# Kernel tuning notes

Measured on AMD Instinct MI355X. Metric: run time of the kernel, lower is better.

Reference implementation:

```python
import jax, jax.numpy as jnp
import numpy as np

HID = 128
NUM_LAYERS = 3
B = 256
ND, ED, SD = 16384, 65536, 131072
NP_, EP, SP = 131072, 524288, 524288


def setup_inputs():
    key = jax.random.key(0)
    ks = jax.random.split(key, 40)
    r = lambda i, sh: jax.random.normal(ks[i], sh, jnp.float32) * 0.05
    ri = lambda i, sh, hi: jax.random.randint(ks[i], sh, 0, hi, jnp.int32)
    return {
        'drug_x': r(0, (ND, 78)),
        'prot_x': r(1, (NP_, 70)),
        'd_feature': r(2, (B, HID)),
        'p_feature': r(3, (B, HID)),
        'drug_edge_index': ri(4, (2, ED), ND),
        'drug_batch': jnp.sort(ri(5, (ND,), B)),
        'drug_sub_node': ri(6, (SD,), ND),
        'drug_sub_ind': ri(7, (SD,), ND),
        'prot_edge_index': ri(8, (2, EP), NP_),
        'prot_batch': jnp.sort(ri(9, (NP_,), B)),
        'prot_sub_node': ri(10, (SP,), NP_),
        'prot_sub_ind': ri(11, (SP,), NP_),
        'enc_Wd': r(12, (78, HID)), 'enc_bd': r(13, (HID,)),
        'enc_Wp': r(14, (70, HID)), 'enc_bp': r(15, (HID,)),
        'convW_d': r(16, (NUM_LAYERS, HID, HID)), 'convb_d': r(17, (NUM_LAYERS, HID)),
        'convW_p': r(18, (NUM_LAYERS, HID, HID)), 'convb_p': r(19, (NUM_LAYERS, HID)),
        'bng_d': jnp.ones((NUM_LAYERS, HID), jnp.float32), 'bnb_d': jnp.zeros((NUM_LAYERS, HID), jnp.float32),
        'bng_p': jnp.ones((NUM_LAYERS, HID), jnp.float32), 'bnb_p': jnp.zeros((NUM_LAYERS, HID), jnp.float32),
        'vn_emb_d': r(20, (HID,)), 'vn_emb_p': r(21, (HID,)),
        'vnW_d': r(22, (NUM_LAYERS - 1, HID, HID)), 'vnb_d': r(23, (NUM_LAYERS - 1, HID)),
        'vnW_p': r(24, (NUM_LAYERS - 1, HID, HID)), 'vnb_p': r(25, (NUM_LAYERS - 1, HID)),
        'mlpd1_W': r(26, (2 * HID, HID)), 'mlpd1_b': r(27, (HID,)),
        'mlpd1_g': jnp.ones((HID,), jnp.float32), 'mlpd1_be': jnp.zeros((HID,), jnp.float32),
        'mlpp1_W': r(28, (2 * HID, HID)), 'mlpp1_b': r(29, (HID,)),
        'mlpp1_g': jnp.ones((HID,), jnp.float32), 'mlpp1_be': jnp.zeros((HID,), jnp.float32),
    }


def _bn(x, g, b):
    # training-mode batch norm (batch statistics)
    m = jnp.mean(x, 0)
    v = jnp.var(x, 0)
    return (x - m) * jax.lax.rsqrt(v + 1e-5) * g + b


def _seg_mean(x, ids, n):
    s = jax.ops.segment_sum(x, ids, num_segments=n)
    c = jax.ops.segment_sum(jnp.ones((x.shape[0],), x.dtype), ids, num_segments=n)
    return s / jnp.maximum(c, 1.0)[:, None]


def _gcn(h, W, b, ei, n):
    # PyG GCNConv: sym-normalized A+I, then linear
    src, dst = ei[0], ei[1]
    hw = h @ W
    deg = jax.ops.segment_sum(jnp.ones((src.shape[0],), h.dtype), dst, num_segments=n) + 1.0
    nrm = jax.lax.rsqrt(deg)
    msg = hw[src] * (nrm[src] * nrm[dst])[:, None]  # [E, HID]
    return jax.ops.segment_sum(msg, dst, num_segments=n) + hw * (nrm * nrm)[:, None] + b


def _forward(fl, ints):
    (drug_x, prot_x, d_feature, p_feature, enc_Wd, enc_bd, enc_Wp, enc_bp,
     convW_d, convb_d, convW_p, convb_p, bng_d, bnb_d, bng_p, bnb_p,
     vn_emb_d, vn_emb_p, vnW_d, vnb_d, vnW_p, vnb_p,
     mlpd1_W, mlpd1_b, mlpd1_g, mlpd1_be, mlpp1_W, mlpp1_b, mlpp1_g, mlpp1_be) = fl
    (d_ei, d_batch, d_sn, d_si, p_ei, p_batch, p_sn, p_si) = ints
    Nd, Npn = drug_x.shape[0], prot_x.shape[0]
    Bn = d_feature.shape[0]
    hd = drug_x @ enc_Wd + enc_bd
    hp = prot_x @ enc_Wp + enc_bp
    # virtual node init: learned embedding + pretrained fingerprint feature
    vx_d = vn_emb_d[None, :] + d_feature  # [B, HID]
    vx_p = vn_emb_p[None, :] + p_feature
    for i in range(NUM_LAYERS):
        # virtual-node broadcast -> GCN -> BN -> ReLU (dropout off / eval)
        hd = _gcn(hd + vx_d[d_batch], convW_d[i], convb_d[i], d_ei, Nd)
        hp = _gcn(hp + vx_p[p_batch], convW_p[i], convb_p[i], p_ei, Npn)
        hd = jax.nn.relu(_bn(hd, bng_d[i], bnb_d[i]))
        hp = jax.nn.relu(_bn(hp, bng_p[i], bnb_p[i]))
        # k-hop subgraph structure extraction (scatter_mean back to nodes)
        hd_struct = _seg_mean(hd[d_sn], d_si, Nd)
        hp_struct = _seg_mean(hp[p_sn], p_si, Npn)
        if i < NUM_LAYERS - 1:
            vx_d = vx_d + jax.nn.relu((jax.ops.segment_sum(hd_struct, d_batch, num_segments=Bn) + vx_d) @ vnW_d[i] + vnb_d[i])
            vx_p = vx_p + jax.nn.relu((jax.ops.segment_sum(hp_struct, p_batch, num_segments=Bn) + vx_p) @ vnW_p[i] + vnb_p[i])
    # cross-modal sync: broadcast pooled drug info onto protein nodes & vice versa
    sync_drug = hp_struct + _seg_mean(hd_struct, d_batch, Bn)[p_batch]  # [Np, HID]
    sync_prot = hd_struct + _seg_mean(hp_struct, p_batch, Bn)[d_batch]  # [Nd, HID]
    final_drug = _bn(jnp.concatenate([_seg_mean(sync_prot, d_batch, Bn), d_feature], 1) @ mlpd1_W + mlpd1_b, mlpd1_g, mlpd1_be)
    final_prot = _bn(jnp.concatenate([_seg_mean(sync_drug, p_batch, Bn), p_feature], 1) @ mlpp1_W + mlpp1_b, mlpp1_g, mlpp1_be)
    return final_drug, final_prot


def reference(drug_x, prot_x, d_feature, p_feature, drug_edge_index, drug_batch,
              drug_sub_node, drug_sub_ind, prot_edge_index, prot_batch,
              prot_sub_node, prot_sub_ind, enc_Wd, enc_bd, enc_Wp, enc_bp,
              convW_d, convb_d, convW_p, convb_p, bng_d, bnb_d, bng_p, bnb_p,
              vn_emb_d, vn_emb_p, vnW_d, vnb_d, vnW_p, vnb_p,
              mlpd1_W, mlpd1_b, mlpd1_g, mlpd1_be, mlpp1_W, mlpp1_b, mlpp1_g, mlpp1_be):
    fl = (drug_x, prot_x, d_feature, p_feature, enc_Wd, enc_bd, enc_Wp, enc_bp,
          convW_d, convb_d, convW_p, convb_p, bng_d, bnb_d, bng_p, bnb_p,
          vn_emb_d, vn_emb_p, vnW_d, vnb_d, vnW_p, vnb_p,
          mlpd1_W, mlpd1_b, mlpd1_g, mlpd1_be, mlpp1_W, mlpp1_b, mlpp1_g, mlpp1_be)
    ints = (drug_edge_index, drug_batch, drug_sub_node, drug_sub_ind,
            prot_edge_index, prot_batch, prot_sub_node, prot_sub_ind)
    return _forward(fl, ints)
```

## Files before the change

### kernel.cpp

```cpp
#include <hip/hip_runtime.h>
#include <cstdint>
#include <cstddef>

#define HID 128

using bf16x8 = __attribute__((ext_vector_type(8))) short;
using f32x4v = __attribute__((ext_vector_type(4))) float;

static __device__ __forceinline__ unsigned short f2b(float x) {
  unsigned int u = __float_as_uint(x);
  unsigned int r = u + 0x7FFFu + ((u >> 16) & 1u);
  return (unsigned short)(r >> 16);
}
static __device__ __forceinline__ float b2f(unsigned short h) {
  return __uint_as_float(((unsigned int)h) << 16);
}

static __device__ __forceinline__ int lowerb(const int* __restrict__ a, int n, int v) {
  int lo = 0, hi = n;
  while (lo < hi) { int m = (lo + hi) >> 1; if (a[m] < v) lo = m + 1; else hi = m; }
  return lo;
}

__global__ void k_hist_all(const int* i0, int n0, int* c0, const int* i1, int n1, int* c1,
                           const int* i2, int n2, int* c2, const int* i3, int n3, int* c3) {
  const int seg = blockIdx.x & 3;
  const int lb = blockIdx.x >> 2;
  const int stride = (gridDim.x >> 2) * blockDim.x;
  const int start = lb * blockDim.x + threadIdx.x;
  const int* idx = seg == 0 ? i0 : seg == 1 ? i1 : seg == 2 ? i2 : i3;
  int* cnt = seg == 0 ? c0 : seg == 1 ? c1 : seg == 2 ? c2 : c3;
  const int n = seg == 0 ? n0 : seg == 1 ? n1 : seg == 2 ? n2 : n3;
  for (int i = start; i < n; i += stride) atomicAdd(&cnt[idx[i]], 1);
}

__global__ void k_nrm_nb(const int* __restrict__ deg_d, float* __restrict__ nrm_d, int ND,
                         const int* __restrict__ deg_p, float* __restrict__ nrm_p, int NP,
                         const int* __restrict__ d_batch, float* __restrict__ nb_d,
                         const int* __restrict__ p_batch, float* __restrict__ nb_p, int B) {
  const int stride = gridDim.x * blockDim.x;
  const int total = ND + NP + 2 * B;
  for (int i = blockIdx.x * blockDim.x + threadIdx.x; i < total; i += stride) {
    if (i < ND) nrm_d[i] = rsqrtf((float)deg_d[i] + 1.0f);
    else if (i < ND + NP) { const int j = i - ND; nrm_p[j] = rsqrtf((float)deg_p[j] + 1.0f); }
    else if (i < ND + NP + B) {
      const int b = i - ND - NP;
      nb_d[b] = (float)(lowerb(d_batch, ND, b + 1) - lowerb(d_batch, ND, b));
    } else {
      const int b = i - ND - NP - B;
      nb_p[b] = (float)(lowerb(p_batch, NP, b + 1) - lowerb(p_batch, NP, b));
    }
  }
}

__global__ __launch_bounds__(256)
void k_scan1_all(const int* c0, int* r0, int n0, int nb0,
                 const int* c1, int* r1, int n1, int nb1,
                 const int* c2, int* r2, int n2, int nb2,
                 const int* c3, int* r3, int n3, int nb3, int* aux) {
  __shared__ int sh[256];
  int b = blockIdx.x, seg = 0;
  if (b >= nb0) { b -= nb0; seg = 1; }
  if (seg == 1 && b >= nb1) { b -= nb1; seg = 2; }
  if (seg == 2 && b >= nb2) { b -= nb2; seg = 3; }
  const int* cnt = seg == 0 ? c0 : seg == 1 ? c1 : seg == 2 ? c2 : c3;
  int* row = seg == 0 ? r0 : seg == 1 ? r1 : seg == 2 ? r2 : r3;
  const int n = seg == 0 ? n0 : seg == 1 ? n1 : seg == 2 ? n2 : n3;
  const int tid = threadIdx.x;
  const int base = b * 1024 + tid * 4;
  int v0 = base + 0 < n ? cnt[base + 0] : 0;
  int v1 = base + 1 < n ? cnt[base + 1] : 0;
  int v2 = base + 2 < n ? cnt[base + 2] : 0;
  int v3 = base + 3 < n ? cnt[base + 3] : 0;
  const int s = v0 + v1 + v2 + v3;
  sh[tid] = s;
  __syncthreads();
  for (int o = 1; o < 256; o <<= 1) {
    const int t = (tid >= o) ? sh[tid - o] : 0;
    __syncthreads();
    sh[tid] += t;
    __syncthreads();
  }
  int excl = sh[tid] - s;
  if (tid == 255) aux[seg * 256 + b] = sh[255];
  if (base + 0 < n) row[base + 0] = excl; excl += v0;
  if (base + 1 < n) row[base + 1] = excl; excl += v1;
  if (base + 2 < n) row[base + 2] = excl; excl += v2;
  if (base + 3 < n) row[base + 3] = excl;
}

__global__ __launch_bounds__(256)
void k_scan2_all(int* aux, int nb0, int nb1, int nb2, int nb3) {
  __shared__ int sh[256];
  const int seg = blockIdx.x;
  const int nb = seg == 0 ? nb0 : seg == 1 ? nb1 : seg == 2 ? nb2 : nb3;
  int* a = aux + seg * 256;
  const int tid = threadIdx.x;
  const int v = tid < nb ? a[tid] : 0;
  sh[tid] = v;
  __syncthreads();
  for (int o = 1; o < 256; o <<= 1) {
    const int t = (tid >= o) ? sh[tid - o] : 0;
    __syncthreads();
    sh[tid] += t;
    __syncthreads();
  }
  if (tid < nb) a[tid] = sh[tid] - v;
}

__global__ __launch_bounds__(256)
void k_scan3_all(int* r0, int n0, int nb0, int t0, int* r1, int n1, int nb1, int t1,
                 int* r2, int n2, int nb2, int t2, int* r3, int n3, int nb3, int t3,
                 const int* aux) {
  int b = blockIdx.x, seg = 0;
  if (b >= nb0) { b -= nb0; seg = 1; }
  if (seg == 1 && b >= nb1) { b -= nb1; seg = 2; }
  if (seg == 2 && b >= nb2) { b -= nb2; seg = 3; }
  int* row = seg == 0 ? r0 : seg == 1 ? r1 : seg == 2 ? r2 : r3;
  const int n = seg == 0 ? n0 : seg == 1 ? n1 : seg == 2 ? n2 : n3;
  const int total = seg == 0 ? t0 : seg == 1 ? t1 : seg == 2 ? t2 : t3;
  const int add = aux[seg * 256 + b];
  const int base = b * 1024 + threadIdx.x * 4;
  #pragma unroll
  for (int k = 0; k < 4; ++k)
    if (base + k < n) row[base + k] += add;
  if (b == 0 && threadIdx.x == 0) row[n] = total;
}

__global__ void k_fill_all(const int* p_src, const int* p_dst, const int* rowE_p, int* curE_p,
                           int* colE_p, float* cofE_p, const float* nrm_p, int EP,
                           const int* d_src, const int* d_dst, const int* rowE_d, int* curE_d,
                           int* colE_d, float* cofE_d, const float* nrm_d, int ED,
                           const int* p_sn, const int* p_si, const int* rowS_p, int* curS_p,
                           int* colS_p, int SP,
                           const int* d_sn, const int* d_si, const int* rowS_d, int* curS_d,
                           int* colS_d, int SD) {
  const int seg = blockIdx.x & 3;
  const int lb = blockIdx.x >> 2;
  const int stride = (gridDim.x >> 2) * blockDim.x;
  const int start = lb * blockDim.x + threadIdx.x;
  if (seg == 0) {
    for (int e = start; e < EP; e += stride) {
      const int d = p_dst[e], s = p_src[e];
      const int pos = rowE_p[d] + atomicAdd(&curE_p[d], 1);
      colE_p[pos] = s;
      cofE_p[pos] = nrm_p[s] * nrm_p[d];
    }
  } else if (seg == 1) {
    for (int e = start; e < ED; e += stride) {
      const int d = d_dst[e], s = d_src[e];
      const int pos = rowE_d[d] + atomicAdd(&curE_d[d], 1);
      colE_d[pos] = s;
      cofE_d[pos] = nrm_d[s] * nrm_d[d];
    }
  } else if (seg == 2) {
    for (int j = start; j < SP; j += stride) {
      const int t = p_si[j];
      const int pos = rowS_p[t] + atomicAdd(&curS_p[t], 1);
      colS_p[pos] = p_sn[j];
    }
  } else {
    for (int j = start; j < SD; j += stride) {
      const int t = d_si[j];
      const int pos = rowS_d[t] + atomicAdd(&curS_d[t], 1);
      colS_d[pos] = d_sn[j];
    }
  }
}

__global__ void k_vx_init_both(const float* __restrict__ emb_d, const float* __restrict__ d_feat,
                               float* __restrict__ vx_d, const float* __restrict__ emb_p,
                               const float* __restrict__ p_feat, float* __restrict__ vx_p,
                               int half) {
  const int stride = gridDim.x * blockDim.x;
  for (int i = blockIdx.x * blockDim.x + threadIdx.x; i < 2 * half; i += stride) {
    if (i < half) vx_d[i] = emb_d[i & (HID - 1)] + d_feat[i];
    else { const int j = i - half; vx_p[j] = emb_p[j & (HID - 1)] + p_feat[j]; }
  }
}

__global__ __launch_bounds__(256)
void k_wcvt_all(const float* __restrict__ convW_d, const float* __restrict__ convW_p,
                const float* __restrict__ enc_Wd, const float* __restrict__ enc_Wp,
                unsigned short* __restrict__ WhiAll, unsigned short* __restrict__ WloAll) {
  const int seg = blockIdx.x >> 5;
  const int lb = blockIdx.x & 31;
  const float* W;
  int K;
  if (seg < 3) { W = convW_d + (size_t)seg * HID * HID; K = 128; }
  else if (seg < 6) { W = convW_p + (size_t)(seg - 3) * HID * HID; K = 128; }
  else if (seg == 6) { W = enc_Wd; K = 78; }
  else { W = enc_Wp; K = 70; }
  unsigned short* Whi = WhiAll + (size_t)seg * HID * HID;
  unsigned short* Wlo = WloAll + (size_t)seg * HID * HID;
  for (int i = lb * 256 + threadIdx.x; i < HID * HID; i += 32 * 256) {
    const int c = i >> 7, k = i & 127;
    const float v = (k < K) ? W[k * HID + c] : 0.f;
    const unsigned short hi = f2b(v);
    Whi[i] = hi;
    Wlo[i] = f2b(v - b2f(hi));
  }
}

__global__ void k_xcvt_both(const float* __restrict__ Xd, int Kd, unsigned short* __restrict__ Dhi,
                            unsigned short* __restrict__ Dlo, int totD,
                            const float* __restrict__ Xp, int Kp, unsigned short* __restrict__ Phi,
                            unsigned short* __restrict__ Plo, int totP) {
  const int stride = gridDim.x * blockDim.x;
  for (int i = blockIdx.x * blockDim.x + threadIdx.x; i < totD + totP; i += stride) {
    if (i < totD) {
      const int node = i >> 7, k = i & 127;
      const float v = (k < Kd) ? Xd[(size_t)node * Kd + k] : 0.f;
      const unsigned short hi = f2b(v);
      Dhi[i] = hi;
      Dlo[i] = f2b(v - b2f(hi));
    } else {
      const int j = i - totD;
      const int node = j >> 7, k = j & 127;
      const float v = (k < Kp) ? Xp[(size_t)node * Kp + k] : 0.f;
      const unsigned short hi = f2b(v);
      Phi[j] = hi;
      Plo[j] = f2b(v - b2f(hi));
    }
  }
}

template<bool ENC>
__global__ __launch_bounds__(256, 2)
void k_gemm_both(const unsigned short* __restrict__ Zhi0, const unsigned short* __restrict__ Zlo0,
                 const unsigned short* __restrict__ Whi0, const unsigned short* __restrict__ Wlo0,
                 const float* __restrict__ bias0, float* __restrict__ G0, int nbk0,
                 const unsigned short* __restrict__ Zhi1, const unsigned short* __restrict__ Zlo1,
                 const unsigned short* __restrict__ Whi1, const unsigned short* __restrict__ Wlo1,
                 const float* __restrict__ bias1, float* __restrict__ G1,
                 float* __restrict__ stats_sl) {
  __shared__ unsigned short Bt[128 * 132];
  __shared__ float lstats[256];
  const int bid = blockIdx.x;
  const bool isP = bid >= nbk0;
  const int lb = isP ? bid - nbk0 : bid;
  const unsigned short* Zhi = isP ? Zhi1 : Zhi0;
  const unsigned short* Zlo = isP ? Zlo1 : Zlo0;
  const unsigned short* Wthi = isP ? Whi1 : Whi0;
  const unsigned short* Wtlo = isP ? Wlo1 : Wlo0;
  const float* bias = isP ? bias1 : bias0;
  float* G = isP ? G1 : G0;

  const int tid = threadIdx.x;
  const int w = tid >> 6;
  const int l = tid & 63;
  const int l15 = l & 15;
  const int kb = l >> 4;

  for (int i = tid; i < 128 * 16; i += 256) {
    const int c = i >> 4, k8 = i & 15;
    *(bf16x8*)(&Bt[c * 132 + k8 * 8]) = *(const bf16x8*)(Wthi + (size_t)c * 128 + k8 * 8);
  }
  if constexpr (!ENC) lstats[tid] = 0.f;

  const int rbase = lb * 128 + w * 32 + l15;
  bf16x8 ahi[2][4], alo[2][4];
  #pragma unroll
  for (int rt = 0; rt < 2; ++rt)
    #pragma unroll
    for (int ks = 0; ks < 4; ++ks) {
      ahi[rt][ks] = *(const bf16x8*)(Zhi + (size_t)(rbase + rt * 16) * 128 + ks * 32 + kb * 8);
      alo[rt][ks] = *(const bf16x8*)(Zlo + (size_t)(rbase + rt * 16) * 128 + ks * 32 + kb * 8);
    }

  f32x4v acc[2][8];
  #pragma unroll
  for (int rt = 0; rt < 2; ++rt)
    #pragma unroll
    for (int ct = 0; ct < 8; ++ct)
      acc[rt][ct] = (f32x4v){0.f, 0.f, 0.f, 0.f};

  __syncthreads();
  #pragma unroll
  for (int ks = 0; ks < 4; ++ks) {
    #pragma unroll
    for (int ct = 0; ct < 8; ++ct) {
      const bf16x8 b = *(const bf16x8*)(&Bt[(ct * 16 + l15) * 132 + ks * 32 + kb * 8]);
      acc[0][ct] = __builtin_amdgcn_mfma_f32_16x16x32_bf16(ahi[0][ks], b, acc[0][ct], 0, 0, 0);
      acc[1][ct] = __builtin_amdgcn_mfma_f32_16x16x32_bf16(ahi[1][ks], b, acc[1][ct], 0, 0, 0);
      acc[0][ct] = __builtin_amdgcn_mfma_f32_16x16x32_bf16(alo[0][ks], b, acc[0][ct], 0, 0, 0);
      acc[1][ct] = __builtin_amdgcn_mfma_f32_16x16x32_bf16(alo[1][ks], b, acc[1][ct], 0, 0, 0);
    }
  }
  __syncthreads();

  for (int i = tid; i < 128 * 16; i += 256) {
    const int c = i >> 4, k8 = i & 15;
    *(bf16x8*)(&Bt[c * 132 + k8 * 8]) = *(const bf16x8*)(Wtlo + (size_t)c * 128 + k8 * 8);
  }
  __syncthreads();
  #pragma unroll
  for (int ks = 0; ks < 4; ++ks) {
    #pragma unroll
    for (int ct = 0; ct < 8; ++ct) {
      const bf16x8 b = *(const bf16x8*)(&Bt[(ct * 16 + l15) * 132 + ks * 32 + kb * 8]);
      acc[0][ct] = __builtin_amdgcn_mfma_f32_16x16x32_bf16(ahi[0][ks], b, acc[0][ct], 0, 0, 0);
      acc[1][ct] = __builtin_amdgcn_mfma_f32_16x16x32_bf16(ahi[1][ks], b, acc[1][ct], 0, 0, 0);
    }
  }

  float bb[8];
  if constexpr (ENC) {
    #pragma unroll
    for (int ct = 0; ct < 8; ++ct) bb[ct] = bias[ct * 16 + l15];
  }
  float csum[8], csq[8];
  #pragma unroll
  for (int ct = 0; ct < 8; ++ct) { csum[ct] = 0.f; csq[ct] = 0.f; }
  #pragma unroll
  for (int rt = 0; rt < 2; ++rt) {
    const size_t grow = (size_t)lb * 128 + w * 32 + rt * 16 + (l >> 4) * 4;
    #pragma unroll
    for (int j = 0; j < 4; ++j) {
      float* gr = G + (grow + j) * 128 + l15;
      #pragma unroll
      for (int ct = 0; ct < 8; ++ct) {
        float v = acc[rt][ct][j];
        if constexpr (ENC) v += bb[ct];
        gr[ct * 16] = v;
        if constexpr (!ENC) { csum[ct] += v; csq[ct] += v * v; }
      }
    }
  }
  if constexpr (!ENC) {
    #pragma unroll
    for (int ct = 0; ct < 8; ++ct) {
      csum[ct] += __shfl_xor(csum[ct], 16);
      csum[ct] += __shfl_xor(csum[ct], 32);
      csq[ct] += __shfl_xor(csq[ct], 16);
      csq[ct] += __shfl_xor(csq[ct], 32);
    }
    if (l < 16) {
      #pragma unroll
      for (int ct = 0; ct < 8; ++ct) {
        atomicAdd(&lstats[ct * 16 + l], csum[ct]);
        atomicAdd(&lstats[128 + ct * 16 + l], csq[ct]);
      }
    }
    __syncthreads();
    const int slice = (isP ? 32 : 0) + (lb & 31);
    atomicAdd(&stats_sl[(size_t)slice * 256 + tid], lstats[tid]);
  }
}

__global__ __launch_bounds__(128)
void k_bn_scale_both(float* __restrict__ stats_sl,
                     const float* g0, const float* b0, float invN0, float* scsh0,
                     const float* g1, const float* b1, float invN1, float* scsh1) {
  const int seg = blockIdx.x;
  float* base = stats_sl + (size_t)seg * 32 * 256;
  const float* g = seg ? g1 : g0;
  const float* bb = seg ? b1 : b0;
  const float invN = seg ? invN1 : invN0;
  float* scsh = seg ? scsh1 : scsh0;
  const int c = threadIdx.x;
  float s = 0.f, ss = 0.f;
  for (int k = 0; k < 32; ++k) {
    s += base[(size_t)k * 256 + c];
    ss += base[(size_t)k * 256 + 128 + c];
    base[(size_t)k * 256 + c] = 0.f;
    base[(size_t)k * 256 + 128 + c] = 0.f;
  }
  const float m = s * invN;
  const float var = ss * invN - m * m;
  const float sc = g[c] * rsqrtf(var + 1e-5f);
  scsh[c] = sc;
  scsh[HID + c] = bb[c] - m * sc;
}

template<bool HASF>
__global__ __launch_bounds__(256)
void k_agg_both(const int* rE0, const int* cE0, const float* wE0, const float* G0,
                const float* scsh0, const int* bat0, const float* vx0, const float* nrm0,
                unsigned short* Zhi0, unsigned short* Zlo0, int nbk0,
                const int* rE1, const int* cE1, const float* wE1, const float* G1,
                const float* scsh1, const int* bat1, const float* vx1, const float* nrm1,
                unsigned short* Zhi1, unsigned short* Zlo1) {
  const int bid = blockIdx.x;
  const bool isP = bid >= nbk0;
  const int lb = isP ? bid - nbk0 : bid;
  const int* rowp = isP ? rE1 : rE0;
  const int* colp = isP ? cE1 : cE0;
  const float* coefp = isP ? wE1 : wE0;
  const float* G = isP ? G1 : G0;
  const float* scsh = isP ? scsh1 : scsh0;
  const int* batch = isP ? bat1 : bat0;
  const float* vx = isP ? vx1 : vx0;
  const float* nrm = isP ? nrm1 : nrm0;
  unsigned short* Zhi = isP ? Zhi1 : Zhi0;
  unsigned short* Zlo = isP ? Zlo1 : Zlo0;

  const int tid = threadIdx.x;
  const int node = lb * 8 + (tid >> 5);
  const int c4 = tid & 31;
  float4 sc, shv;
  if constexpr (HASF) {
    sc = ((const float4*)scsh)[c4];
    shv = ((const float4*)(scsh + HID))[c4];
  }
  auto loadU = [&](int i) -> float4 {
    float4 v = *(const float4*)(G + (size_t)i * HID + c4 * 4);
    if constexpr (HASF) {
      v.x = fmaxf(v.x * sc.x + shv.x, 0.f);
      v.y = fmaxf(v.y * sc.y + shv.y, 0.f);
      v.z = fmaxf(v.z * sc.z + shv.z, 0.f);
      v.w = fmaxf(v.w * sc.w + shv.w, 0.f);
    }
    const float4 u = *(const float4*)(vx + (size_t)batch[i] * HID + c4 * 4);
    v.x += u.x; v.y += u.y; v.z += u.z; v.w += u.w;
    return v;
  };
  const int lo = rowp[node], hi = rowp[node + 1];
  const float nv = nrm[node];
  const float s2 = nv * nv;
  float4 acc = loadU(node);
  acc.x *= s2; acc.y *= s2; acc.z *= s2; acc.w *= s2;
  int e = lo;
  for (; e + 4 <= hi; e += 4) {
    const float w0 = coefp[e], w1 = coefp[e + 1], w2 = coefp[e + 2], w3 = coefp[e + 3];
    const float4 v0 = loadU(colp[e]);
    const float4 v1 = loadU(colp[e + 1]);
    const float4 v2 = loadU(colp[e + 2]);
    const float4 v3 = loadU(colp[e + 3]);
    acc.x += v0.x * w0 + v1.x * w1 + v2.x * w2 + v3.x * w3;
    acc.y += v0.y * w0 + v1.y * w1 + v2.y * w2 + v3.y * w3;
    acc.z += v0.z * w0 + v1.z * w1 + v2.z * w2 + v3.z * w3;
    acc.w += v0.w * w0 + v1.w * w1 + v2.w * w2 + v3.w * w3;
  }
  for (; e < hi; ++e) {
    const float w = coefp[e];
    const float4 v = loadU(colp[e]);
    acc.x += v.x * w; acc.y += v.y * w; acc.z += v.z * w; acc.w += v.w * w;
  }
  ushort4 h, lo4;
  h.x = f2b(acc.x); lo4.x = f2b(acc.x - b2f(h.x));
  h.y = f2b(acc.y); lo4.y = f2b(acc.y - b2f(h.y));
  h.z = f2b(acc.z); lo4.z = f2b(acc.z - b2f(h.z));
  h.w = f2b(acc.w); lo4.w = f2b(acc.w - b2f(h.w));
  *(ushort4*)(Zhi + (size_t)node * HID + c4 * 4) = h;
  *(ushort4*)(Zlo + (size_t)node * HID + c4 * 4) = lo4;
}

__global__ __launch_bounds__(256)
void k_sub_pool_both(const int* rS0, const int* cS0, const float* G0, const float* scsh0,
                     const int* bat0, float* sumS0, int nbk0,
                     const int* rS1, const int* cS1, const float* G1, const float* scsh1,
                     const int* bat1, float* sumS1) {
  __shared__ float sh[8][HID];
  __shared__ int batl[8];
  const int bid = blockIdx.x;
  const bool isP = bid >= nbk0;
  const int lb = isP ? bid - nbk0 : bid;
  const int* rowp = isP ? rS1 : rS0;
  const int* colp = isP ? cS1 : cS0;
  const float* G = isP ? G1 : G0;
  const float* scsh = isP ? scsh1 : scsh0;
  const int* batch = isP ? bat1 : bat0;
  float* sumS = isP ? sumS1 : sumS0;

  const int tid = threadIdx.x;
  const int grp = tid >> 5;
  const int node = lb * 8 + grp;
  const int c4 = tid & 31;
  const float4 sc = ((const float4*)scsh)[c4];
  const float4 shv = ((const float4*)(scsh + HID))[c4];
  const int lo = rowp[node], hi = rowp[node + 1];
  float4 acc = {0.f, 0.f, 0.f, 0.f};
  int e = lo;
  for (; e + 4 <= hi; e += 4) {
    const int i0 = colp[e], i1 = colp[e + 1], i2 = colp[e + 2], i3 = colp[e + 3];
    const float4 v0 = *(const float4*)(G + (size_t)i0 * HID + c4 * 4);
    const float4 v1 = *(const float4*)(G + (size_t)i1 * HID + c4 * 4);
    const float4 v2 = *(const float4*)(G + (size_t)i2 * HID + c4 * 4);
    const float4 v3 = *(const float4*)(G + (size_t)i3 * HID + c4 * 4);
    acc.x += fmaxf(v0.x * sc.x + shv.x, 0.f) + fmaxf(v1.x * sc.x + shv.x, 0.f)
           + fmaxf(v2.x * sc.x + shv.x, 0.f) + fmaxf(v3.x * sc.x + shv.x, 0.f);
    acc.y += fmaxf(v0.y * sc.y + shv.y, 0.f) + fmaxf(v1.y * sc.y + shv.y, 0.f)
           + fmaxf(v2.y * sc.y + shv.y, 0.f) + fmaxf(v3.y * sc.y + shv.y, 0.f);
    acc.z += fmaxf(v0.z * sc.z + shv.z, 0.f) + fmaxf(v1.z * sc.z + shv.z, 0.f)
           + fmaxf(v2.z * sc.z + shv.z, 0.f) + fmaxf(v3.z * sc.z + shv.z, 0.f);
    acc.w += fmaxf(v0.w * sc.w + shv.w, 0.f) + fmaxf(v1.w * sc.w + shv.w, 0.f)
           + fmaxf(v2.w * sc.w + shv.w, 0.f) + fmaxf(v3.w * sc.w + shv.w, 0.f);
  }
  for (; e < hi; ++e) {
    const float4 v = *(const float4*)(G + (size_t)colp[e] * HID + c4 * 4);
    acc.x += fmaxf(v.x * sc.x + shv.x, 0.f);
    acc.y += fmaxf(v.y * sc.y + shv.y, 0.f);
    acc.z += fmaxf(v.z * sc.z + shv.z, 0.f);
    acc.w += fmaxf(v.w * sc.w + shv.w, 0.f);
  }
  const float inv = 1.0f / fmaxf((float)(hi - lo), 1.0f);
  acc.x *= inv; acc.y *= inv; acc.z *= inv; acc.w *= inv;
  ((float4*)&sh[grp][0])[c4] = acc;
  if (tid < 8) batl[tid] = batch[lb * 8 + tid];
  __syncthreads();
  if (tid < HID) {
    int cur = batl[0];
    float a = 0.f;
    #pragma unroll
    for (int g = 0; g < 8; ++g) {
      if (batl[g] != cur) {
        atomicAdd(&sumS[(size_t)cur * HID + tid], a);
        a = 0.f;
        cur = batl[g];
      }
      a += sh[g][tid];
    }
    atomicAdd(&sumS[(size_t)cur * HID + tid], a);
  }
}

__global__ __launch_bounds__(128)
void k_vn_update_both(const float* ps0, float* vx0, const float* W0, const float* b0,
                      const float* ps1, float* vx1, const float* W1, const float* b1, int B) {
  const int gb = blockIdx.x;
  const bool isP = gb >= B;
  const int b = isP ? gb - B : gb;
  const float* pooledSum = isP ? ps1 : ps0;
  float* vx = isP ? vx1 : vx0;
  const float* W = isP ? W1 : W0;
  const float* bias = isP ? b1 : b0;
  const int c = threadIdx.x;
  __shared__ float xin[HID];
  xin[c] = pooledSum[(size_t)b * HID + c] + vx[(size_t)b * HID + c];
  __syncthreads();
  float acc = bias[c];
  #pragma unroll 8
  for (int k = 0; k < HID; k += 4) {
    const float4 x = *(const float4*)&xin[k];
    acc += x.x * W[k * HID + c] + x.y * W[(k + 1) * HID + c]
         + x.z * W[(k + 2) * HID + c] + x.w * W[(k + 3) * HID + c];
  }
  vx[(size_t)b * HID + c] += fmaxf(acc, 0.0f);
}

__global__ __launch_bounds__(128)
void k_final_A(const float* __restrict__ sum_Sd, const float* __restrict__ sum_Sp,
               const float* __restrict__ nb_d, const float* __restrict__ nb_p,
               float* __restrict__ A_d, float* __restrict__ A_p) {
  const int b = blockIdx.x, c = threadIdx.x;
  const float nd = nb_d[b], np_ = nb_p[b];
  const float md = sum_Sd[(size_t)b * HID + c] / fmaxf(nd, 1.f);
  const float mp = sum_Sp[(size_t)b * HID + c] / fmaxf(np_, 1.f);
  A_d[(size_t)b * HID + c] = md + (nd > 0.f ? mp : 0.f);
  A_p[(size_t)b * HID + c] = mp + (np_ > 0.f ? md : 0.f);
}

__global__ __launch_bounds__(128)
void k_final_mlp_both(const float* A0, const float* f0, const float* W0, const float* b0,
                      const float* A1, const float* f1, const float* W1, const float* b1,
                      float* __restrict__ fpre, int B) {
  const int gb = blockIdx.x;
  const bool isP = gb >= B;
  const int b = isP ? gb - B : gb;
  const float* A = isP ? A1 : A0;
  const float* feat = isP ? f1 : f0;
  const float* W = isP ? W1 : W0;
  const float* bias = isP ? b1 : b0;
  const int c = threadIdx.x;
  __shared__ float xin[2 * HID];
  xin[c] = A[(size_t)b * HID + c];
  xin[HID + c] = feat[(size_t)b * HID + c];
  __syncthreads();
  float acc = bias[c];
  #pragma unroll 8
  for (int k = 0; k < 2 * HID; k += 4) {
    const float4 x = *(const float4*)&xin[k];
    acc += x.x * W[k * HID + c] + x.y * W[(k + 1) * HID + c]
         + x.z * W[(k + 2) * HID + c] + x.w * W[(k + 3) * HID + c];
  }
  fpre[(size_t)gb * HID + c] = acc;
}

__global__ __launch_bounds__(256)
void k_bn_stats_both(const float* __restrict__ fpre, float* __restrict__ statsF, int B) {
  __shared__ float sh[2][256];
  const int seg = blockIdx.x >= 128 ? 1 : 0;
  const int lb = blockIdx.x - seg * 128;
  const float* X = fpre + (size_t)seg * B * HID;
  float* stats = statsF + seg * 256;
  const int tid = threadIdx.x;
  const int c = tid & (HID - 1);
  const int half = tid >> 7;
  float s = 0.f, ss = 0.f;
  for (int r = lb * 2 + half; r < B; r += 256) {
    const float v = X[(size_t)r * HID + c];
    s += v; ss += v * v;
  }
  sh[0][tid] = s; sh[1][tid] = ss;
  __syncthreads();
  if (tid < HID) {
    atomicAdd(&stats[c], sh[0][tid] + sh[0][tid + 128]);
    atomicAdd(&stats[HID + c], sh[1][tid] + sh[1][tid + 128]);
  }
}

__global__ void k_bn_apply_both(const float* __restrict__ fpre, float* __restrict__ out,
                                const float* __restrict__ statsF,
                                const float* g0, const float* b0,
                                const float* g1, const float* b1, int B, float invN) {
  const int stride = gridDim.x * blockDim.x;
  const int n4 = 2 * B * 32;
  for (int i = blockIdx.x * blockDim.x + threadIdx.x; i < n4; i += stride) {
    const int seg = i >= B * 32 ? 1 : 0;
    const int c4 = i & 31;
    const float* stats = statsF + seg * 256;
    const float4 m4 = ((const float4*)stats)[c4];
    const float4 q4 = ((const float4*)stats)[32 + c4];
    const float4 g4 = ((const float4*)(seg ? g1 : g0))[c4];
    const float4 b4 = ((const float4*)(seg ? b1 : b0))[c4];
    float4 v = ((const float4*)fpre)[i];
    float m, va;
    m = m4.x * invN; va = q4.x * invN - m * m; v.x = (v.x - m) * rsqrtf(va + 1e-5f) * g4.x + b4.x;
    m = m4.y * invN; va = q4.y * invN - m * m; v.y = (v.y - m) * rsqrtf(va + 1e-5f) * g4.y + b4.y;
    m = m4.z * invN; va = q4.z * invN - m * m; v.z = (v.z - m) * rsqrtf(va + 1e-5f) * g4.z + b4.z;
    m = m4.w * invN; va = q4.w * invN - m * m; v.w = (v.w - m) * rsqrtf(va + 1e-5f) * g4.w + b4.w;
    ((float4*)out)[i] = v;
  }
}

extern "C" void kernel_launch(void* const* d_in, const int* in_sizes, int n_in,
                              void* d_out, int out_size, void* d_ws, size_t ws_size,
                              hipStream_t stream) {
  const float* drug_x   = (const float*)d_in[0];
  const float* prot_x   = (const float*)d_in[1];
  const float* d_feat   = (const float*)d_in[2];
  const float* p_feat   = (const float*)d_in[3];
  const int*   d_ei     = (const int*)d_in[4];
  const int*   d_batch  = (const int*)d_in[5];
  const int*   d_sn     = (const int*)d_in[6];
  const int*   d_si     = (const int*)d_in[7];
  const int*   p_ei     = (const int*)d_in[8];
  const int*   p_batch  = (const int*)d_in[9];
  const int*   p_sn     = (const int*)d_in[10];
  const int*   p_si     = (const int*)d_in[11];
  const float* enc_Wd   = (const float*)d_in[12];
  const float* enc_bd   = (const float*)d_in[13];
  const float* enc_Wp   = (const float*)d_in[14];
  const float* enc_bp   = (const float*)d_in[15];
  const float* convW_d  = (const float*)d_in[16];
  const float* convW_p  = (const float*)d_in[18];
  const float* bng_d    = (const float*)d_in[20];
  const float* bnb_d    = (const float*)d_in[21];
  const float* bng_p    = (const float*)d_in[22];
  const float* bnb_p    = (const float*)d_in[23];
  const float* vn_emb_d = (const float*)d_in[24];
  const float* vn_emb_p = (const float*)d_in[25];
  const float* vnW_d    = (const float*)d_in[26];
  const float* vnb_d    = (const float*)d_in[27];
  const float* vnW_p    = (const float*)d_in[28];
  const float* vnb_p    = (const float*)d_in[29];
  const float* mlpd1_W  = (const float*)d_in[30];
  const float* mlpd1_b  = (const float*)d_in[31];
  const float* mlpd1_g  = (const float*)d_in[32];
  const float* mlpd1_be = (const float*)d_in[33];
  const float* mlpp1_W  = (const float*)d_in[34];
  const float* mlpp1_b  = (const float*)d_in[35];
  const float* mlpp1_g  = (const float*)d_in[36];
  const float* mlpp1_be = (const float*)d_in[37];

  const int ND = in_sizes[5];
  const int ED = in_sizes[4] / 2;
  const int SD = in_sizes[6];
  const int NP = in_sizes[9];
  const int EP = in_sizes[8] / 2;
  const int SP = in_sizes[10];
  const int B  = in_sizes[2] / HID;
  (void)n_in; (void)out_size; (void)ws_size;

  char* wsb = (char*)d_ws;
  size_t off = 0;
  auto alloc = [&](size_t bytes) -> void* {
    void* p = (void*)(wsb + off);
    off = (off + bytes + 255) & ~(size_t)255;
    return p;
  };
  float* Gp = (float*)alloc((size_t)NP * HID * 4);
  unsigned short* Zhi_p = (unsigned short*)alloc((size_t)NP * HID * 2);
  unsigned short* Zlo_p = (unsigned short*)alloc((size_t)NP * HID * 2);
  float* Gd = (float*)alloc((size_t)ND * HID * 4);
  unsigned short* Zhi_d = (unsigned short*)alloc((size_t)ND * HID * 2);
  unsigned short* Zlo_d = (unsigned short*)alloc((size_t)ND * HID * 2);
  unsigned short* WhiAll = (unsigned short*)alloc((size_t)8 * HID * HID * 2);
  unsigned short* WloAll = (unsigned short*)alloc((size_t)8 * HID * HID * 2);
  float* nrm_p = (float*)alloc((size_t)NP * 4);
  float* nrm_d = (float*)alloc((size_t)ND * 4);
  int* rowE_p = (int*)alloc((size_t)(NP + 1) * 4);
  int* rowE_d = (int*)alloc((size_t)(ND + 1) * 4);
  int* rowS_p = (int*)alloc((size_t)(NP + 1) * 4);
  int* rowS_d = (int*)alloc((size_t)(ND + 1) * 4);
  int* colE_p = (int*)alloc((size_t)EP * 4);
  float* cofE_p = (float*)alloc((size_t)EP * 4);
  int* colE_d = (int*)alloc((size_t)ED * 4);
  float* cofE_d = (float*)alloc((size_t)ED * 4);
  int* colS_p = (int*)alloc((size_t)SP * 4);
  int* colS_d = (int*)alloc((size_t)SD * 4);
  int* aux    = (int*)alloc(4 * 256 * 4);
  float* vx_d  = (float*)alloc((size_t)B * HID * 4);
  float* vx_p  = (float*)alloc((size_t)B * HID * 4);
  float* sum_Sd = (float*)alloc((size_t)B * HID * 4);
  float* sum_Sp = (float*)alloc((size_t)B * HID * 4);
  float* A_d   = (float*)alloc((size_t)B * HID * 4);
  float* A_p   = (float*)alloc((size_t)B * HID * 4);
  float* nb_d  = (float*)alloc((size_t)B * 4);
  float* nb_p  = (float*)alloc((size_t)B * 4);
  float* scsh_d = (float*)alloc(2 * HID * 4);
  float* scsh_p = (float*)alloc(2 * HID * 4);
  float* fpre  = (float*)alloc((size_t)2 * B * HID * 4);
  float* statsF = (float*)alloc(2 * 256 * 4);
  const size_t zstart = off;
  int* deg_p  = (int*)alloc((size_t)NP * 4);
  int* deg_d  = (int*)alloc((size_t)ND * 4);
  int* scnt_p = (int*)alloc((size_t)NP * 4);
  int* scnt_d = (int*)alloc((size_t)ND * 4);
  int* curE_p = (int*)alloc((size_t)NP * 4);
  int* curE_d = (int*)alloc((size_t)ND * 4);
  int* curS_p = (int*)alloc((size_t)NP * 4);
  int* curS_d = (int*)alloc((size_t)ND * 4);
  float* stats_sl = (float*)alloc((size_t)64 * 256 * 4);
  const size_t zend = off;

  const int* d_src = d_ei;  const int* d_dst = d_ei + ED;
  const int* p_src = p_ei;  const int* p_dst = p_ei + EP;

  hipMemsetAsync(wsb + zstart, 0, zend - zstart, stream);
  k_hist_all<<<4096, 256, 0, stream>>>(p_dst, EP, deg_p, d_dst, ED, deg_d,
                                       p_si, SP, scnt_p, d_si, SD, scnt_d);
  k_nrm_nb<<<1024, 256, 0, stream>>>(deg_d, nrm_d, ND, deg_p, nrm_p, NP,
                                     d_batch, nb_d, p_batch, nb_p, B);
  const int nbP = (NP + 1023) / 1024, nbD = (ND + 1023) / 1024;
  k_scan1_all<<<2 * nbP + 2 * nbD, 256, 0, stream>>>(
      deg_p, rowE_p, NP, nbP, deg_d, rowE_d, ND, nbD,
      scnt_p, rowS_p, NP, nbP, scnt_d, rowS_d, ND, nbD, aux);
  k_scan2_all<<<4, 256, 0, stream>>>(aux, nbP, nbD, nbP, nbD);
  k_scan3_all<<<2 * nbP + 2 * nbD, 256, 0, stream>>>(
      rowE_p, NP, nbP, EP, rowE_d, ND, nbD, ED,
      rowS_p, NP, nbP, SP, rowS_d, ND, nbD, SD, aux);
  k_fill_all<<<4096, 256, 0, stream>>>(
      p_src, p_dst, rowE_p, curE_p, colE_p, cofE_p, nrm_p, EP,
      d_src, d_dst, rowE_d, curE_d, colE_d, cofE_d, nrm_d, ED,
      p_sn, p_si, rowS_p, curS_p, colS_p, SP,
      d_sn, d_si, rowS_d, curS_d, colS_d, SD);

  k_wcvt_all<<<256, 256, 0, stream>>>(convW_d, convW_p, enc_Wd, enc_Wp, WhiAll, WloAll);
  k_xcvt_both<<<4096, 256, 0, stream>>>(drug_x, 78, Zhi_d, Zlo_d, ND * HID,
                                        prot_x, 70, Zhi_p, Zlo_p, NP * HID);
  k_gemm_both<true><<<ND / 128 + NP / 128, 256, 0, stream>>>(
      Zhi_d, Zlo_d, WhiAll + (size_t)6 * HID * HID, WloAll + (size_t)6 * HID * HID,
      enc_bd, Gd, ND / 128,
      Zhi_p, Zlo_p, WhiAll + (size_t)7 * HID * HID, WloAll + (size_t)7 * HID * HID,
      enc_bp, Gp, nullptr);
  k_vx_init_both<<<128, 256, 0, stream>>>(vn_emb_d, d_feat, vx_d, vn_emb_p, p_feat, vx_p, B * HID);

  for (int l = 0; l < 3; ++l) {
    if (l == 0)
      k_agg_both<false><<<ND / 8 + NP / 8, 256, 0, stream>>>(
          rowE_d, colE_d, cofE_d, Gd, nullptr, d_batch, vx_d, nrm_d, Zhi_d, Zlo_d, ND / 8,
          rowE_p, colE_p, cofE_p, Gp, nullptr, p_batch, vx_p, nrm_p, Zhi_p, Zlo_p);
    else
      k_agg_both<true><<<ND / 8 + NP / 8, 256, 0, stream>>>(
          rowE_d, colE_d, cofE_d, Gd, scsh_d, d_batch, vx_d, nrm_d, Zhi_d, Zlo_d, ND / 8,
          rowE_p, colE_p, cofE_p, Gp, scsh_p, p_batch, vx_p, nrm_p, Zhi_p, Zlo_p);
    k_gemm_both<false><<<ND / 128 + NP / 128, 256, 0, stream>>>(
        Zhi_d, Zlo_d, WhiAll + (size_t)l * HID * HID, WloAll + (size_t)l * HID * HID,
        nullptr, Gd, ND / 128,
        Zhi_p, Zlo_p, WhiAll + (size_t)(3 + l) * HID * HID, WloAll + (size_t)(3 + l) * HID * HID,
        nullptr, Gp, stats_sl);
    k_bn_scale_both<<<2, 128, 0, stream>>>(stats_sl,
        bng_d + l * HID, bnb_d + l * HID, 1.0f / (float)ND, scsh_d,
        bng_p + l * HID, bnb_p + l * HID, 1.0f / (float)NP, scsh_p);
    hipMemsetAsync(sum_Sd, 0, (size_t)2 * B * HID * 4, stream);
    k_sub_pool_both<<<ND / 8 + NP / 8, 256, 0, stream>>>(
        rowS_d, colS_d, Gd, scsh_d, d_batch, sum_Sd, ND / 8,
        rowS_p, colS_p, Gp, scsh_p, p_batch, sum_Sp);
    if (l < 2)
      k_vn_update_both<<<2 * B, 128, 0, stream>>>(
          sum_Sd, vx_d, vnW_d + (size_t)l * HID * HID, vnb_d + l * HID,
          sum_Sp, vx_p, vnW_p + (size_t)l * HID * HID, vnb_p + l * HID, B);
  }

  k_final_A<<<B, 128, 0, stream>>>(sum_Sd, sum_Sp, nb_d, nb_p, A_d, A_p);
  k_final_mlp_both<<<2 * B, 128, 0, stream>>>(A_d, d_feat, mlpd1_W, mlpd1_b,
                                              A_p, p_feat, mlpp1_W, mlpp1_b, fpre, B);
  hipMemsetAsync(statsF, 0, 2 * 256 * 4, stream);
  k_bn_stats_both<<<256, 256, 0, stream>>>(fpre, statsF, B);
  k_bn_apply_both<<<128, 256, 0, stream>>>(fpre, (float*)d_out, statsF,
                                           mlpd1_g, mlpd1_be, mlpp1_g, mlpp1_be,
                                           B, 1.0f / (float)B);
}
```

Measured before the change: 719.7 us.

## Fuse prep kernels, drop subgraph CSR, pool subgraphs via flat LDS atomics

Merges the histogram, input and weight bf16 split conversion, and virtual-node init into one launch, so fewer small kernels run during preprocessing. Removes the subgraph CSR build (scan and fill) and replaces the per-node sub-pool with a flat pass over subgraph entries. That pass accumulates relu(BN(G))/count into a per-block 256x128 shared-memory buffer with LDS atomics, then flushes it to global with atomics. Edge coefficients are now computed on the fly from nrm instead of being stored, and the sum buffer zeroing moves into the BN scale kernel. In exchange there are heavy LDS atomic contention, a large shared-memory footprint with only one block per CU, and a float summation order that is no longer deterministic.

After: 1.933 ms. 2.69x slower.

```diff
diff --git a/kernel.cpp b/kernel.cpp
--- a/kernel.cpp
+++ b/kernel.cpp
@@ -3,6 +3,8 @@
 #include <cstddef>
 
 #define HID 128
+#define HB 1024
+#define XB 2048
 
 using bf16x8 = __attribute__((ext_vector_type(8))) short;
 using f32x4v = __attribute__((ext_vector_type(4))) float;
@@ -22,32 +24,88 @@
   return lo;
 }
 
-__global__ void k_hist_all(const int* i0, int n0, int* c0, const int* i1, int n1, int* c1,
-                           const int* i2, int n2, int* c2, const int* i3, int n3, int* c3) {
-  const int seg = blockIdx.x & 3;
-  const int lb = blockIdx.x >> 2;
-  const int stride = (gridDim.x >> 2) * blockDim.x;
-  const int start = lb * blockDim.x + threadIdx.x;
-  const int* idx = seg == 0 ? i0 : seg == 1 ? i1 : seg == 2 ? i2 : i3;
-  int* cnt = seg == 0 ? c0 : seg == 1 ? c1 : seg == 2 ? c2 : c3;
-  const int n = seg == 0 ? n0 : seg == 1 ? n1 : seg == 2 ? n2 : n3;
-  for (int i = start; i < n; i += stride) atomicAdd(&cnt[idx[i]], 1);
-}
-
-__global__ void k_nrm_nb(const int* __restrict__ deg_d, float* __restrict__ nrm_d, int ND,
-                         const int* __restrict__ deg_p, float* __restrict__ nrm_p, int NP,
-                         const int* __restrict__ d_batch, float* __restrict__ nb_d,
-                         const int* __restrict__ p_batch, float* __restrict__ nb_p, int B) {
+__global__ __launch_bounds__(256)
+void k_prep1(const int* p_dst, int EP, int* deg_p, const int* d_dst, int ED, int* deg_d,
+             const int* p_si, int SP, int* scnt_p, const int* d_si, int SD, int* scnt_d,
+             const float* Xd, int Kd, unsigned short* Dhi, unsigned short* Dlo, int totD,
+             const float* Xp, int Kp, unsigned short* Phi, unsigned short* Plo, int totP,
+             const float* convW_d, const float* convW_p,
+             const float* enc_Wd, const float* enc_Wp,
+             unsigned short* WhiAll, unsigned short* WloAll,
+             const float* emb_d, const float* d_feat, float* vx_d,
+             const float* emb_p, const float* p_feat, float* vx_p, int vhalf) {
+  const int b = blockIdx.x;
+  const int tid = threadIdx.x;
+  if (b < 4 * HB) {
+    const int seg = b & 3, lb = b >> 2;
+    const int stride = HB * 256;
+    const int* idx = seg == 0 ? p_dst : seg == 1 ? d_dst : seg == 2 ? p_si : d_si;
+    int* cnt = seg == 0 ? deg_p : seg == 1 ? deg_d : seg == 2 ? scnt_p : scnt_d;
+    const int n = seg == 0 ? EP : seg == 1 ? ED : seg == 2 ? SP : SD;
+    for (int i = lb * 256 + tid; i < n; i += stride) atomicAdd(&cnt[idx[i]], 1);
+  } else if (b < 4 * HB + XB) {
+    const int lb = b - 4 * HB;
+    for (int i = lb * 256 + tid; i < totD + totP; i += XB * 256) {
+      if (i < totD) {
+        const int node = i >> 7, k = i & 127;
+        const float v = (k < Kd) ? Xd[(size_t)node * Kd + k] : 0.f;
+        const unsigned short hi = f2b(v);
+        Dhi[i] = hi;
+        Dlo[i] = f2b(v - b2f(hi));
+      } else {
+        const int j = i - totD;
+        const int node = j >> 7, k = j & 127;
+        const float v = (k < Kp) ? Xp[(size_t)node * Kp + k] : 0.f;
+        const unsigned short hi = f2b(v);
+        Phi[j] = hi;
+        Plo[j] = f2b(v - b2f(hi));
+      }
+    }
+  } else if (b < 4 * HB + XB + 256) {
+    const int lb = b - (4 * HB + XB);
+    const int seg = lb >> 5;
+    const float* W;
+    int K;
+    if (seg < 3) { W = convW_d + (size_t)seg * HID * HID; K = 128; }
+    else if (seg < 6) { W = convW_p + (size_t)(seg - 3) * HID * HID; K = 128; }
+    else if (seg == 6) { W = enc_Wd; K = 78; }
+    else { W = enc_Wp; K = 70; }
+    unsigned short* Whi = WhiAll + (size_t)seg * HID * HID;
+    unsigned short* Wlo = WloAll + (size_t)seg * HID * HID;
+    for (int i = (lb & 31) * 256 + tid; i < HID * HID; i += 32 * 256) {
+      const int c = i >> 7, k = i & 127;
+      const float v = (k < K) ? W[k * HID + c] : 0.f;
+      const unsigned short hi = f2b(v);
+      Whi[i] = hi;
+      Wlo[i] = f2b(v - b2f(hi));
+    }
+  } else {
+    const int lb = b - (4 * HB + XB + 256);
+    for (int i = lb * 256 + tid; i < 2 * vhalf; i += 128 * 256) {
+      if (i < vhalf) vx_d[i] = emb_d[i & (HID - 1)] + d_feat[i];
+      else { const int j = i - vhalf; vx_p[j] = emb_p[j & (HID - 1)] + p_feat[j]; }
+    }
+  }
+}
+
+__global__ void k_nrm_inb(const int* deg_d, float* nrm_d, int ND,
+                          const int* deg_p, float* nrm_p, int NP,
+                          const int* scnt_d, float* invc_d,
+                          const int* scnt_p, float* invc_p,
+                          const int* d_batch, float* nb_d,
+                          const int* p_batch, float* nb_p, int B) {
   const int stride = gridDim.x * blockDim.x;
-  const int total = ND + NP + 2 * B;
+  const int total = 2 * ND + 2 * NP + 2 * B;
   for (int i = blockIdx.x * blockDim.x + threadIdx.x; i < total; i += stride) {
     if (i < ND) nrm_d[i] = rsqrtf((float)deg_d[i] + 1.0f);
     else if (i < ND + NP) { const int j = i - ND; nrm_p[j] = rsqrtf((float)deg_p[j] + 1.0f); }
-    else if (i < ND + NP + B) {
-      const int b = i - ND - NP;
+    else if (i < 2 * ND + NP) { const int j = i - ND - NP; invc_d[j] = 1.0f / fmaxf((float)scnt_d[j], 1.f); }
+    else if (i < 2 * ND + 2 * NP) { const int j = i - 2 * ND - NP; invc_p[j] = 1.0f / fmaxf((float)scnt_p[j], 1.f); }
+    else if (i < 2 * ND + 2 * NP + B) {
+      const int b = i - 2 * ND - 2 * NP;
       nb_d[b] = (float)(lowerb(d_batch, ND, b + 1) - lowerb(d_batch, ND, b));
     } else {
-      const int b = i - ND - NP - B;
+      const int b = i - 2 * ND - 2 * NP - B;
       nb_p[b] = (float)(lowerb(p_batch, NP, b + 1) - lowerb(p_batch, NP, b));
     }
   }
@@ -55,17 +113,13 @@
 
 __global__ __launch_bounds__(256)
 void k_scan1_all(const int* c0, int* r0, int n0, int nb0,
-                 const int* c1, int* r1, int n1, int nb1,
-                 const int* c2, int* r2, int n2, int nb2,
-                 const int* c3, int* r3, int n3, int nb3, int* aux) {
+                 const int* c1, int* r1, int n1, int nb1, int* aux) {
   __shared__ int sh[256];
   int b = blockIdx.x, seg = 0;
   if (b >= nb0) { b -= nb0; seg = 1; }
-  if (seg == 1 && b >= nb1) { b -= nb1; seg = 2; }
-  if (seg == 2 && b >= nb2) { b -= nb2; seg = 3; }
-  const int* cnt = seg == 0 ? c0 : seg == 1 ? c1 : seg == 2 ? c2 : c3;
-  int* row = seg == 0 ? r0 : seg == 1 ? r1 : seg == 2 ? r2 : r3;
-  const int n = seg == 0 ? n0 : seg == 1 ? n1 : seg == 2 ? n2 : n3;
+  const int* cnt = seg == 0 ? c0 : c1;
+  int* row = seg == 0 ? r0 : r1;
+  const int n = seg == 0 ? n0 : n1;
   const int tid = threadIdx.x;
   const int base = b * 1024 + tid * 4;
   int v0 = base + 0 < n ? cnt[base + 0] : 0;
@@ -90,10 +144,10 @@
 }
 
 __global__ __launch_bounds__(256)
-void k_scan2_all(int* aux, int nb0, int nb1, int nb2, int nb3) {
+void k_scan2_all(int* aux, int nb0, int nb1) {
   __shared__ int sh[256];
   const int seg = blockIdx.x;
-  const int nb = seg == 0 ? nb0 : seg == 1 ? nb1 : seg == 2 ? nb2 : nb3;
+  const int nb = seg == 0 ? nb0 : nb1;
   int* a = aux + seg * 256;
   const int tid = threadIdx.x;
   const int v = tid < nb ? a[tid] : 0;
@@ -109,16 +163,13 @@
 }
 
 __global__ __launch_bounds__(256)
-void k_scan3_all(int* r0, int n0, int nb0, int t0, int* r1, int n1, int nb1, int t1,
-                 int* r2, int n2, int nb2, int t2, int* r3, int n3, int nb3, int t3,
-                 const int* aux) {
+void k_scan3_all(int* r0, int n0, int nb0, int t0,
+                 int* r1, int n1, int nb1, int t1, const int* aux) {
   int b = blockIdx.x, seg = 0;
   if (b >= nb0) { b -= nb0; seg = 1; }
-  if (seg == 1 && b >= nb1) { b -= nb1; seg = 2; }
-  if (seg == 2 && b >= nb2) { b -= nb2; seg = 3; }
-  int* row = seg == 0 ? r0 : seg == 1 ? r1 : seg == 2 ? r2 : r3;
-  const int n = seg == 0 ? n0 : seg == 1 ? n1 : seg == 2 ? n2 : n3;
-  const int total = seg == 0 ? t0 : seg == 1 ? t1 : seg == 2 ? t2 : t3;
+  int* row = seg == 0 ? r0 : r1;
+  const int n = seg == 0 ? n0 : n1;
+  const int total = seg == 0 ? t0 : t1;
   const int add = aux[seg * 256 + b];
   const int base = b * 1024 + threadIdx.x * 4;
   #pragma unroll
@@ -127,101 +178,24 @@
   if (b == 0 && threadIdx.x == 0) row[n] = total;
 }
 
-__global__ void k_fill_all(const int* p_src, const int* p_dst, const int* rowE_p, int* curE_p,
-                           int* colE_p, float* cofE_p, const float* nrm_p, int EP,
-                           const int* d_src, const int* d_dst, const int* rowE_d, int* curE_d,
-                           int* colE_d, float* cofE_d, const float* nrm_d, int ED,
-                           const int* p_sn, const int* p_si, const int* rowS_p, int* curS_p,
-                           int* colS_p, int SP,
-                           const int* d_sn, const int* d_si, const int* rowS_d, int* curS_d,
-                           int* colS_d, int SD) {
-  const int seg = blockIdx.x & 3;
-  const int lb = blockIdx.x >> 2;
-  const int stride = (gridDim.x >> 2) * blockDim.x;
+__global__ void k_fill_e(const int* p_src, const int* p_dst, const int* rowE_p, int* curE_p,
+                         int* colE_p, int EP,
+                         const int* d_src, const int* d_dst, const int* rowE_d, int* curE_d,
+                         int* colE_d, int ED) {
+  const int seg = blockIdx.x & 1;
+  const int lb = blockIdx.x >> 1;
+  const int stride = (gridDim.x >> 1) * blockDim.x;
   const int start = lb * blockDim.x + threadIdx.x;
-  if (seg == 0) {
-    for (int e = start; e < EP; e += stride) {
-      const int d = p_dst[e], s = p_src[e];
-      const int pos = rowE_p[d] + atomicAdd(&curE_p[d], 1);
-      colE_p[pos] = s;
-      cofE_p[pos] = nrm_p[s] * nrm_p[d];
-    }
-  } else if (seg == 1) {
-    for (int e = start; e < ED; e += stride) {
-      const int d = d_dst[e], s = d_src[e];
-      const int pos = rowE_d[d] + atomicAdd(&curE_d[d], 1);
-      colE_d[pos] = s;
-      cofE_d[pos] = nrm_d[s] * nrm_d[d];
-    }
-  } else if (seg == 2) {
-    for (int j = start; j < SP; j += stride) {
-      const int t = p_si[j];
-      const int pos = rowS_p[t] + atomicAdd(&curS_p[t], 1);
-      colS_p[pos] = p_sn[j];
-    }
-  } else {
-    for (int j = start; j < SD; j += stride) {
-      const int t = d_si[j];
-      const int pos = rowS_d[t] + atomicAdd(&curS_d[t], 1);
-      colS_d[pos] = d_sn[j];
-    }
-  }
-}
-
-__global__ void k_vx_init_both(const float* __restrict__ emb_d, const float* __restrict__ d_feat,
-                               float* __restrict__ vx_d, const float* __restrict__ emb_p,
-                               const float* __restrict__ p_feat, float* __restrict__ vx_p,
-                               int half) {
-  const int stride = gridDim.x * blockDim.x;
-  for (int i = blockIdx.x * blockDim.x + threadIdx.x; i < 2 * half; i += stride) {
-    if (i < half) vx_d[i] = emb_d[i & (HID - 1)] + d_feat[i];
-    else { const int j = i - half; vx_p[j] = emb_p[j & (HID - 1)] + p_feat[j]; }
-  }
-}
-
-__global__ __launch_bounds__(256)
-void k_wcvt_all(const float* __restrict__ convW_d, const float* __restrict__ convW_p,
-                const float* __restrict__ enc_Wd, const float* __restrict__ enc_Wp,
-                unsigned short* __restrict__ WhiAll, unsigned short* __restrict__ WloAll) {
-  const int seg = blockIdx.x >> 5;
-  const int lb = blockIdx.x & 31;
-  const float* W;
-  int K;
-  if (seg < 3) { W = convW_d + (size_t)seg * HID * HID; K = 128; }
-  else if (seg < 6) { W = convW_p + (size_t)(seg - 3) * HID * HID; K = 128; }
-  else if (seg == 6) { W = enc_Wd; K = 78; }
-  else { W = enc_Wp; K = 70; }
-  unsigned short* Whi = WhiAll + (size_t)seg * HID * HID;
-  unsigned short* Wlo = WloAll + (size_t)seg * HID * HID;
-  for (int i = lb * 256 + threadIdx.x; i < HID * HID; i += 32 * 256) {
-    const int c = i >> 7, k = i & 127;
-    const float v = (k < K) ? W[k * HID + c] : 0.f;
-    const unsigned short hi = f2b(v);
-    Whi[i] = hi;
-    Wlo[i] = f2b(v - b2f(hi));
-  }
-}
-
-__global__ void k_xcvt_both(const float* __restrict__ Xd, int Kd, unsigned short* __restrict__ Dhi,
-                            unsigned short* __restrict__ Dlo, int totD,
-                            const float* __restrict__ Xp, int Kp, unsigned short* __restrict__ Phi,
-                            unsigned short* __restrict__ Plo, int totP) {
-  const int stride = gridDim.x * blockDim.x;
-  for (int i = blockIdx.x * blockDim.x + threadIdx.x; i < totD + totP; i += stride) {
-    if (i < totD) {
-      const int node = i >> 7, k = i & 127;
-      const float v = (k < Kd) ? Xd[(size_t)node * Kd + k] : 0.f;
-      const unsigned short hi = f2b(v);
-      Dhi[i] = hi;
-      Dlo[i] = f2b(v - b2f(hi));
-    } else {
-      const int j = i - totD;
-      const int node = j >> 7, k = j & 127;
-      const float v = (k < Kp) ? Xp[(size_t)node * Kp + k] : 0.f;
-      const unsigned short hi = f2b(v);
-      Phi[j] = hi;
-      Plo[j] = f2b(v - b2f(hi));
-    }
+  const int* src = seg ? d_src : p_src;
+  const int* dst = seg ? d_dst : p_dst;
+  const int* row = seg ? rowE_d : rowE_p;
+  int* cur = seg ? curE_d : curE_p;
+  int* col = seg ? colE_d : colE_p;
+  const int E = seg ? ED : EP;
+  for (int e = start; e < E; e += stride) {
+    const int d = dst[e];
+    const int pos = row[d] + atomicAdd(&cur[d], 1);
+    col[pos] = src[e];
   }
 }
 
@@ -350,14 +324,16 @@
 
 __global__ __launch_bounds__(128)
 void k_bn_scale_both(float* __restrict__ stats_sl,
-                     const float* g0, const float* b0, float invN0, float* scsh0,
-                     const float* g1, const float* b1, float invN1, float* scsh1) {
+                     const float* g0, const float* b0, float invN0, float* scsh0, float* zero0,
+                     const float* g1, const float* b1, float invN1, float* scsh1, float* zero1,
+                     int zn4) {
   const int seg = blockIdx.x;
   float* base = stats_sl + (size_t)seg * 32 * 256;
   const float* g = seg ? g1 : g0;
   const float* bb = seg ? b1 : b0;
   const float invN = seg ? invN1 : invN0;
   float* scsh = seg ? scsh1 : scsh0;
+  float* zero = seg ? zero1 : zero0;
   const int c = threadIdx.x;
   float s = 0.f, ss = 0.f;
   for (int k = 0; k < 32; ++k) {
@@ -371,14 +347,16 @@
   const float sc = g[c] * rsqrtf(var + 1e-5f);
   scsh[c] = sc;
   scsh[HID + c] = bb[c] - m * sc;
+  const float4 z = {0.f, 0.f, 0.f, 0.f};
+  for (int i = c; i < zn4; i += 128) ((float4*)zero)[i] = z;
 }
 
 template<bool HASF>
 __global__ __launch_bounds__(256)
-void k_agg_both(const int* rE0, const int* cE0, const float* wE0, const float* G0,
+void k_agg_both(const int* rE0, const int* cE0, const float* G0,
                 const float* scsh0, const int* bat0, const float* vx0, const float* nrm0,
                 unsigned short* Zhi0, unsigned short* Zlo0, int nbk0,
-                const int* rE1, const int* cE1, const float* wE1, const float* G1,
+                const int* rE1, const int* cE1, const float* G1,
                 const float* scsh1, const int* bat1, const float* vx1, const float* nrm1,
                 unsigned short* Zhi1, unsigned short* Zlo1) {
   const int bid = blockIdx.x;
@@ -386,7 +364,6 @@
   const int lb = isP ? bid - nbk0 : bid;
   const int* rowp = isP ? rE1 : rE0;
   const int* colp = isP ? cE1 : cE0;
-  const float* coefp = isP ? wE1 : wE0;
   const float* G = isP ? G1 : G0;
   const float* scsh = isP ? scsh1 : scsh0;
   const int* batch = isP ? bat1 : bat0;
@@ -422,19 +399,21 @@
   acc.x *= s2; acc.y *= s2; acc.z *= s2; acc.w *= s2;
   int e = lo;
   for (; e + 4 <= hi; e += 4) {
-    const float w0 = coefp[e], w1 = coefp[e + 1], w2 = coefp[e + 2], w3 = coefp[e + 3];
-    const float4 v0 = loadU(colp[e]);
-    const float4 v1 = loadU(colp[e + 1]);
-    const float4 v2 = loadU(colp[e + 2]);
-    const float4 v3 = loadU(colp[e + 3]);
+    const int i0 = colp[e], i1 = colp[e + 1], i2 = colp[e + 2], i3 = colp[e + 3];
+    const float w0 = nrm[i0] * nv, w1 = nrm[i1] * nv, w2 = nrm[i2] * nv, w3 = nrm[i3] * nv;
+    const float4 v0 = loadU(i0);
+    const float4 v1 = loadU(i1);
+    const float4 v2 = loadU(i2);
+    const float4 v3 = loadU(i3);
     acc.x += v0.x * w0 + v1.x * w1 + v2.x * w2 + v3.x * w3;
     acc.y += v0.y * w0 + v1.y * w1 + v2.y * w2 + v3.y * w3;
     acc.z += v0.z * w0 + v1.z * w1 + v2.z * w2 + v3.z * w3;
     acc.w += v0.w * w0 + v1.w * w1 + v2.w * w2 + v3.w * w3;
   }
   for (; e < hi; ++e) {
-    const float w = coefp[e];
-    const float4 v = loadU(colp[e]);
+    const int i0 = colp[e];
+    const float w = nrm[i0] * nv;
+    const float4 v = loadU(i0);
     acc.x += v.x * w; acc.y += v.y * w; acc.z += v.z * w; acc.w += v.w * w;
   }
   ushort4 h, lo4;
@@ -446,72 +425,53 @@
   *(ushort4*)(Zlo + (size_t)node * HID + c4 * 4) = lo4;
 }
 
-__global__ __launch_bounds__(256)
-void k_sub_pool_both(const int* rS0, const int* cS0, const float* G0, const float* scsh0,
-                     const int* bat0, float* sumS0, int nbk0,
-                     const int* rS1, const int* cS1, const float* G1, const float* scsh1,
-                     const int* bat1, float* sumS1) {
-  __shared__ float sh[8][HID];
-  __shared__ int batl[8];
+__global__ __launch_bounds__(1024, 1)
+void k_sub_flat(const int* sn_p, const int* si_p, const float* Gp, const float* scsh_p,
+                const int* bat_p, const float* invc_p, float* sumS_p, int SP, int PB,
+                const int* sn_d, const int* si_d, const float* Gd, const float* scsh_d,
+                const int* bat_d, const float* invc_d, float* sumS_d, int SD, int DB, int B) {
+  __shared__ float lacc[256 * HID];
   const int bid = blockIdx.x;
-  const bool isP = bid >= nbk0;
-  const int lb = isP ? bid - nbk0 : bid;
-  const int* rowp = isP ? rS1 : rS0;
-  const int* colp = isP ? cS1 : cS0;
-  const float* G = isP ? G1 : G0;
-  const float* scsh = isP ? scsh1 : scsh0;
-  const int* batch = isP ? bat1 : bat0;
-  float* sumS = isP ? sumS1 : sumS0;
-
-  const int tid = threadIdx.x;
-  const int grp = tid >> 5;
-  const int node = lb * 8 + grp;
-  const int c4 = tid & 31;
-  const float4 sc = ((const float4*)scsh)[c4];
-  const float4 shv = ((const float4*)(scsh + HID))[c4];
-  const int lo = rowp[node], hi = rowp[node + 1];
-  float4 acc = {0.f, 0.f, 0.f, 0.f};
-  int e = lo;
-  for (; e + 4 <= hi; e += 4) {
-    const int i0 = colp[e], i1 = colp[e + 1], i2 = colp[e + 2], i3 = colp[e + 3];
-    const float4 v0 = *(const float4*)(G + (size_t)i0 * HID + c4 * 4);
-    const float4 v1 = *(const float4*)(G + (size_t)i1 * HID + c4 * 4);
-    const float4 v2 = *(const float4*)(G + (size_t)i2 * HID + c4 * 4);
-    const float4 v3 = *(const float4*)(G + (size_t)i3 * HID + c4 * 4);
-    acc.x += fmaxf(v0.x * sc.x + shv.x, 0.f) + fmaxf(v1.x * sc.x + shv.x, 0.f)
-           + fmaxf(v2.x * sc.x + shv.x, 0.f) + fmaxf(v3.x * sc.x + shv.x, 0.f);
-    acc.y += fmaxf(v0.y * sc.y + shv.y, 0.f) + fmaxf(v1.y * sc.y + shv.y, 0.f)
-           + fmaxf(v2.y * sc.y + shv.y, 0.f) + fmaxf(v3.y * sc.y + shv.y, 0.f);
-    acc.z += fmaxf(v0.z * sc.z + shv.z, 0.f) + fmaxf(v1.z * sc.z + shv.z, 0.f)
-           + fmaxf(v2.z * sc.z + shv.z, 0.f) + fmaxf(v3.z * sc.z + shv.z, 0.f);
-    acc.w += fmaxf(v0.w * sc.w + shv.w, 0.f) + fmaxf(v1.w * sc.w + shv.w, 0.f)
-           + fmaxf(v2.w * sc.w + shv.w, 0.f) + fmaxf(v3.w * sc.w + shv.w, 0.f);
-  }
-  for (; e < hi; ++e) {
-    const float4 v = *(const float4*)(G + (size_t)colp[e] * HID + c4 * 4);
-    acc.x += fmaxf(v.x * sc.x + shv.x, 0.f);
-    acc.y += fmaxf(v.y * sc.y + shv.y, 0.f);
-    acc.z += fmaxf(v.z * sc.z + shv.z, 0.f);
-    acc.w += fmaxf(v.w * sc.w + shv.w, 0.f);
-  }
-  const float inv = 1.0f / fmaxf((float)(hi - lo), 1.0f);
-  acc.x *= inv; acc.y *= inv; acc.z *= inv; acc.w *= inv;
-  ((float4*)&sh[grp][0])[c4] = acc;
-  if (tid < 8) batl[tid] = batch[lb * 8 + tid];
-  __syncthreads();
-  if (tid < HID) {
-    int cur = batl[0];
-    float a = 0.f;
+  const bool isD = bid >= PB;
+  const int lb = isD ? bid - PB : bid;
+  const int nblk = isD ? DB : PB;
+  const int SC = isD ? SD : SP;
+  const int* sn = isD ? sn_d : sn_p;
+  const int* si = isD ? si_d : si_p;
+  const float* G = isD ? Gd : Gp;
+  const float* scsh = isD ? scsh_d : scsh_p;
+  const int* bat = isD ? bat_d : bat_p;
+  const float* invc = isD ? invc_d : invc_p;
+  float* sumS = isD ? sumS_d : sumS_p;
+
+  for (int i = threadIdx.x; i < 256 * HID; i += 1024) lacc[i] = 0.f;
+  const int g = threadIdx.x >> 5;
+  const int c = threadIdx.x & 31;
+  float scv[4], shv[4];
+  #pragma unroll
+  for (int k = 0; k < 4; ++k) { scv[k] = scsh[c + 32 * k]; shv[k] = scsh[HID + c + 32 * k]; }
+  __syncthreads();
+
+  const int chunk = (SC + nblk - 1) / nblk;
+  const int jend = min((lb + 1) * chunk, SC);
+  for (int j = lb * chunk + g; j < jend; j += 32) {
+    const int node = sn[j];
+    const int tgt = si[j];
+    const float ic = invc[tgt];
+    const int bb = bat[tgt];
+    const float* gr = G + (size_t)node * HID;
+    float* dst = &lacc[bb * HID];
     #pragma unroll
-    for (int g = 0; g < 8; ++g) {
-      if (batl[g] != cur) {
-        atomicAdd(&sumS[(size_t)cur * HID + tid], a);
-        a = 0.f;
-        cur = batl[g];
-      }
-      a += sh[g][tid];
-    }
-    atomicAdd(&sumS[(size_t)cur * HID + tid], a);
+    for (int k = 0; k < 4; ++k) {
+      const int ch = c + 32 * k;
+      const float v = fmaxf(gr[ch] * scv[k] + shv[k], 0.f) * ic;
+      atomicAdd(&dst[ch], v);
+    }
+  }
+  __syncthreads();
+  for (int i = threadIdx.x; i < B * HID; i += 1024) {
+    const float v = lacc[i];
+    if (v != 0.f) atomicAdd(&sumS[i], v);
   }
 }
 
@@ -690,17 +650,13 @@
   unsigned short* WloAll = (unsigned short*)alloc((size_t)8 * HID * HID * 2);
   float* nrm_p = (float*)alloc((size_t)NP * 4);
   float* nrm_d = (float*)alloc((size_t)ND * 4);
+  float* invc_p = (float*)alloc((size_t)NP * 4);
+  float* invc_d = (float*)alloc((size_t)ND * 4);
   int* rowE_p = (int*)alloc((size_t)(NP + 1) * 4);
   int* rowE_d = (int*)alloc((size_t)(ND + 1) * 4);
-  int* rowS_p = (int*)alloc((size_t)(NP + 1) * 4);
-  int* rowS_d = (int*)alloc((size_t)(ND + 1) * 4);
   int* colE_p = (int*)alloc((size_t)EP * 4);
-  float* cofE_p = (float*)alloc((size_t)EP * 4);
   int* colE_d = (int*)alloc((size_t)ED * 4);
-  float* cofE_d = (float*)alloc((size_t)ED * 4);
-  int* colS_p = (int*)alloc((size_t)SP * 4);
-  int* colS_d = (int*)alloc((size_t)SD * 4);
-  int* aux    = (int*)alloc(4 * 256 * 4);
+  int* aux    = (int*)alloc(2 * 256 * 4);
   float* vx_d  = (float*)alloc((size_t)B * HID * 4);
   float* vx_p  = (float*)alloc((size_t)B * HID * 4);
   float* sum_Sd = (float*)alloc((size_t)B * HID * 4);
@@ -720,8 +676,6 @@
   int* scnt_d = (int*)alloc((size_t)ND * 4);
   int* curE_p = (int*)alloc((size_t)NP * 4);
   int* curE_d = (int*)alloc((size_t)ND * 4);
-  int* curS_p = (int*)alloc((size_t)NP * 4);
-  int* curS_d = (int*)alloc((size_t)ND * 4);
   float* stats_sl = (float*)alloc((size_t)64 * 256 * 4);
   const size_t zend = off;
 
@@ -729,55 +683,49 @@
   const int* p_src = p_ei;  const int* p_dst = p_ei + EP;
 
   hipMemsetAsync(wsb + zstart, 0, zend - zstart, stream);
-  k_hist_all<<<4096, 256, 0, stream>>>(p_dst, EP, deg_p, d_dst, ED, deg_d,
-                                       p_si, SP, scnt_p, d_si, SD, scnt_d);
-  k_nrm_nb<<<1024, 256, 0, stream>>>(deg_d, nrm_d, ND, deg_p, nrm_p, NP,
-                                     d_batch, nb_d, p_batch, nb_p, B);
+  k_prep1<<<4 * HB + XB + 256 + 128, 256, 0, stream>>>(
+      p_dst, EP, deg_p, d_dst, ED, deg_d, p_si, SP, scnt_p, d_si, SD, scnt_d,
+      drug_x, 78, Zhi_d, Zlo_d, ND * HID, prot_x, 70, Zhi_p, Zlo_p, NP * HID,
+      convW_d, convW_p, enc_Wd, enc_Wp, WhiAll, WloAll,
+      vn_emb_d, d_feat, vx_d, vn_emb_p, p_feat, vx_p, B * HID);
+  k_nrm_inb<<<1024, 256, 0, stream>>>(deg_d, nrm_d, ND, deg_p, nrm_p, NP,
+                                      scnt_d, invc_d, scnt_p, invc_p,
+                                      d_batch, nb_d, p_batch, nb_p, B);
   const int nbP = (NP + 1023) / 1024, nbD = (ND + 1023) / 1024;
-  k_scan1_all<<<2 * nbP + 2 * nbD, 256, 0, stream>>>(
-      deg_p, rowE_p, NP, nbP, deg_d, rowE_d, ND, nbD,
-      scnt_p, rowS_p, NP, nbP, scnt_d, rowS_d, ND, nbD, aux);
-  k_scan2_all<<<4, 256, 0, stream>>>(aux, nbP, nbD, nbP, nbD);
-  k_scan3_all<<<2 * nbP + 2 * nbD, 256, 0, stream>>>(
-      rowE_p, NP, nbP, EP, rowE_d, ND, nbD, ED,
-      rowS_p, NP, nbP, SP, rowS_d, ND, nbD, SD, aux);
-  k_fill_all<<<4096, 256, 0, stream>>>(
-      p_src, p_dst, rowE_p, curE_p, colE_p, cofE_p, nrm_p, EP,
-      d_src, d_dst, rowE_d, curE_d, colE_d, cofE_d, nrm_d, ED,
-      p_sn, p_si, rowS_p, curS_p, colS_p, SP,
-      d_sn, d_si, rowS_d, curS_d, colS_d, SD);
-
-  k_wcvt_all<<<256, 256, 0, stream>>>(convW_d, convW_p, enc_Wd, enc_Wp, WhiAll, WloAll);
-  k_xcvt_both<<<4096, 256, 0, stream>>>(drug_x, 78, Zhi_d, Zlo_d, ND * HID,
-                                        prot_x, 70, Zhi_p, Zlo_p, NP * HID);
+  k_scan1_all<<<nbP + nbD, 256, 0, stream>>>(deg_p, rowE_p, NP, nbP, deg_d, rowE_d, ND, nbD, aux);
+  k_scan2_all<<<2, 256, 0, stream>>>(aux, nbP, nbD);
+  k_scan3_all<<<nbP + nbD, 256, 0, stream>>>(rowE_p, NP, nbP, EP, rowE_d, ND, nbD, ED, aux);
+  k_fill_e<<<4096, 256, 0, stream>>>(p_src, p_dst, rowE_p, curE_p, colE_p, EP,
+                                     d_src, d_dst, rowE_d, curE_d, colE_d, ED);
+
   k_gemm_both<true><<<ND / 128 + NP / 128, 256, 0, stream>>>(
       Zhi_d, Zlo_d, WhiAll + (size_t)6 * HID * HID, WloAll + (size_t)6 * HID * HID,
       enc_bd, Gd, ND / 128,
       Zhi_p, Zlo_p, WhiAll + (size_t)7 * HID * HID, WloAll + (size_t)7 * HID * HID,
       enc_bp, Gp, nullptr);
-  k_vx_init_both<<<128, 256, 0, stream>>>(vn_emb_d, d_feat, vx_d, vn_emb_p, p_feat, vx_p, B * HID);
-
+
+  const int PB = 208, DB = 48;
   for (int l = 0; l < 3; ++l) {
     if (l == 0)
       k_agg_both<false><<<ND / 8 + NP / 8, 256, 0, stream>>>(
-          rowE_d, colE_d, cofE_d, Gd, nullptr, d_batch, vx_d, nrm_d, Zhi_d, Zlo_d, ND / 8,
-          rowE_p, colE_p, cofE_p, Gp, nullptr, p_batch, vx_p, nrm_p, Zhi_p, Zlo_p);
+          rowE_d, colE_d, Gd, nullptr, d_batch, vx_d, nrm_d, Zhi_d, Zlo_d, ND / 8,
+          rowE_p, colE_p, Gp, nullptr, p_batch, vx_p, nrm_p, Zhi_p, Zlo_p);
     else
       k_agg_both<true><<<ND / 8 + NP / 8, 256, 0, stream>>>(
-          rowE_d, colE_d, cofE_d, Gd, scsh_d, d_batch, vx_d, nrm_d, Zhi_d, Zlo_d, ND / 8,
-          rowE_p, colE_p, cofE_p, Gp, scsh_p, p_batch, vx_p, nrm_p, Zhi_p, Zlo_p);
+          rowE_d, colE_d, Gd, scsh_d, d_batch, vx_d, nrm_d, Zhi_d, Zlo_d, ND / 8,
+          rowE_p, colE_p, Gp, scsh_p, p_batch, vx_p, nrm_p, Zhi_p, Zlo_p);
     k_gemm_both<false><<<ND / 128 + NP / 128, 256, 0, stream>>>(
         Zhi_d, Zlo_d, WhiAll + (size_t)l * HID * HID, WloAll + (size_t)l * HID * HID,
         nullptr, Gd, ND / 128,
         Zhi_p, Zlo_p, WhiAll + (size_t)(3 + l) * HID * HID, WloAll + (size_t)(3 + l) * HID * HID,
         nullptr, Gp, stats_sl);
     k_bn_scale_both<<<2, 128, 0, stream>>>(stats_sl,
-        bng_d + l * HID, bnb_d + l * HID, 1.0f / (float)ND, scsh_d,
-        bng_p + l * HID, bnb_p + l * HID, 1.0f / (float)NP, scsh_p);
-    hipMemsetAsync(sum_Sd, 0, (size_t)2 * B * HID * 4, stream);
-    k_sub_pool_both<<<ND / 8 + NP / 8, 256, 0, stream>>>(
-        rowS_d, colS_d, Gd, scsh_d, d_batch, sum_Sd, ND / 8,
-        rowS_p, colS_p, Gp, scsh_p, p_batch, sum_Sp);
+        bng_d + l * HID, bnb_d + l * HID, 1.0f / (float)ND, scsh_d, sum_Sd,
+        bng_p + l * HID, bnb_p + l * HID, 1.0f / (float)NP, scsh_p, sum_Sp,
+        B * HID / 4);
+    k_sub_flat<<<PB + DB, 1024, 0, stream>>>(
+        p_sn, p_si, Gp, scsh_p, p_batch, invc_p, sum_Sp, SP, PB,
+        d_sn, d_si, Gd, scsh_d, d_batch, invc_d, sum_Sd, SD, DB, B);
     if (l < 2)
       k_vn_update_both<<<2 * B, 128, 0, stream>>>(
           sum_Sd, vx_d, vnW_d + (size_t)l * HID * HID, vnb_d + l * HID,
```
